# Performance work log

Hardware: AMD Instinct MI355X
Metric: run time of the kernel (lower is better)

Reference implementation:

```python
import jax, jax.numpy as jnp
import numpy as np

NEG_BIG = -9e15
ALPHA = 0.2  # LeakyReLU slope


def setup_inputs() -> dict:
    key = jax.random.key(0)
    k1, k2, k3, k4 = jax.random.split(key, 4)
    B, N, Fin, Fout = 8, 2048, 256, 64
    h = jax.random.normal(k1, (B, N, Fin), dtype=jnp.float32)
    adj = jax.random.randint(k2, (B, N, N), 0, 2, dtype=jnp.int32)
    # xavier_uniform-ish scale for W and a
    W = jax.random.normal(k3, (Fin, Fout), dtype=jnp.float32) * (1.414 * np.sqrt(2.0 / (Fin + Fout)))
    a = jax.random.normal(k4, (2 * Fout, 1), dtype=jnp.float32) * (1.414 * np.sqrt(2.0 / (2 * Fout + 1)))
    return {"h": h, "adj": adj, "W": W, "a": a}


def reference(h, adj, W, a):
    Fout = W.shape[1]
    Wh = jnp.einsum("bnf,fo->bno", h, W)  # [B,N,Fout]
    # Decompose concat-based score: a_input @ a == Wh@a1 (src) + Wh@a2 (dst)
    a1, a2 = a[:Fout, 0], a[Fout:, 0]
    e_src = Wh @ a1  # [B,N]
    e_dst = Wh @ a2  # [B,N]
    e = e_src[:, :, None] + e_dst[:, None, :]  # [B,N,N]
    e = jnp.where(e > 0, e, ALPHA * e)  # LeakyReLU
    scores = jnp.where(adj > 0, e, NEG_BIG)
    attention = jax.nn.softmax(scores, axis=-1)  # [B,N,N]
    h_prime = jnp.einsum("bnm,bmo->bno", attention, Wh)
    return jax.nn.elu(h_prime)  # concat=True
```

## Files before the change

### kernel.cpp

```cpp
#include <hip/hip_runtime.h>

#define L2E 1.44269504088896340736f

typedef float f32x4 __attribute__((ext_vector_type(4)));
typedef __bf16 bf16x8 __attribute__((ext_vector_type(8)));
typedef __bf16 bf16x4 __attribute__((ext_vector_type(4)));

__device__ inline void mfma_bf16(bf16x8 a, bf16x8 b, f32x4& c) {
    c = __builtin_amdgcn_mfma_f32_16x16x32_bf16(a, b, c, 0, 0, 0);
}


__global__ __launch_bounds__(256, 2)
void k1_wh(const float* __restrict__ h, const float* __restrict__ W,
           const float* __restrict__ a, __bf16* __restrict__ whP,
           float* __restrict__ esrc, float* __restrict__ edst) {
    const int tid  = threadIdx.x;
    const int lane = tid & 63;
    const int w    = tid >> 6;
    const int blk  = blockIdx.x;
    const int r0   = blk * 8;
    const int b    = r0 >> 11;
    const int n0   = r0 & 2047;

    __shared__ float pt_s[8][4][64];
    __shared__ float whs[64][8];

    float wreg[64];
    {
        const float* Wp = W + (size_t)(w * 64) * 64 + lane;
#pragma unroll
        for (int kk = 0; kk < 64; kk++) wreg[kk] = Wp[(size_t)kk * 64];
    }

    const float* hbase = h + (size_t)r0 * 256 + w * 64;
    for (int rr = 0; rr < 8; rr++) {
        const float4* hp = (const float4*)(hbase + rr * 256);
        float acc = 0.f;
#pragma unroll
        for (int q = 0; q < 16; q++) {
            float4 hv = hp[q];
            acc += hv.x * wreg[4 * q + 0];
            acc += hv.y * wreg[4 * q + 1];
            acc += hv.z * wreg[4 * q + 2];
            acc += hv.w * wreg[4 * q + 3];
        }
        pt_s[rr][w][lane] = acc;
    }
    __syncthreads();

    const float a1 = a[lane];
    const float a2 = a[64 + lane];
#pragma unroll
    for (int rq = 0; rq < 2; rq++) {
        const int rr = w * 2 + rq;
        float v = pt_s[rr][0][lane] + pt_s[rr][1][lane] +
                  pt_s[rr][2][lane] + pt_s[rr][3][lane];
        whs[lane][rr] = v;
        float e1 = v * a1, e2 = v * a2;
#pragma unroll
        for (int d = 1; d < 64; d <<= 1) {
            e1 += __shfl_xor(e1, d);
            e2 += __shfl_xor(e2, d);
        }
        if (lane == 0) { esrc[r0 + rr] = e1; edst[r0 + rr] = e2; }
    }
    __syncthreads();

    if (tid < 128) {
        const int o  = tid >> 1, hf = (tid & 1) * 4;
        float4 v = *(const float4*)&whs[o][hf];
        bf16x4 bv = { (__bf16)v.x, (__bf16)v.y, (__bf16)v.z, (__bf16)v.w };
        const int t   = n0 >> 6;
        const int kh  = (n0 >> 5) & 1;
        const int hi2 = (n0 >> 3) & 3;
        const int ob  = o >> 4;
        const int rr  = o & 15;
        const size_t flat =
            ((((size_t)(b * 32 + t) * 2 + kh) * 4 + ob) * 4 + hi2) * 128 +
            rr * 8 + hf;
        *(bf16x4*)(whP + flat) = bv;
    }
}

__global__ __launch_bounds__(256, 2)
void k2_attn(const int* __restrict__ adj, const __bf16* __restrict__ whP,
             const float* __restrict__ esrc, const float* __restrict__ edst,
             float* __restrict__ out) {
    const int tid  = threadIdx.x;
    const int lane = tid & 63;
    const int jg   = tid >> 6;
    const int blk  = blockIdx.x;
    const int b    = blk >> 7;
    const int i0   = (blk & 127) * 16;
    const int r    = lane & 15;
    const int hi   = lane >> 4;

    __shared__ float edst_s[2048];
    __shared__ float esrc_s[16];
    __shared__ float red_s[4];
    __shared__ unsigned msk_s[16][66];
    __shared__ float mrg_acc[3][1024];
    __shared__ float mrg_l[3][16];

#pragma unroll
    for (int rr = 0; rr < 4; rr++) {
        const int row = jg * 4 + rr;
        const int* arow = adj + (size_t)(b * 2048 + i0 + row) * 2048 + lane;
        int av[32];
#pragma unroll
        for (int k = 0; k < 32; k++) av[k] = arow[k * 64];
        unsigned myd = 0u;
#pragma unroll
        for (int k = 0; k < 32; k++) {
            unsigned long long bal = __ballot(av[k] > 0);
            if ((lane >> 1) == k)
                myd = (lane & 1) ? (unsigned)(bal >> 32) : (unsigned)bal;
        }
        msk_s[row][lane] = myd;
    }

    float mymax = -3.0e38f;
#pragma unroll
    for (int q = 0; q < 2; q++) {
        float4 v = *(const float4*)&edst[b * 2048 + q * 1024 + tid * 4];
        *(float4*)&edst_s[q * 1024 + tid * 4] = v;
        mymax = fmaxf(fmaxf(mymax, v.x), fmaxf(v.y, fmaxf(v.z, v.w)));
    }
#pragma unroll
    for (int d = 1; d < 64; d <<= 1) mymax = fmaxf(mymax, __shfl_xor(mymax, d));
    if (lane == 0) red_s[jg] = mymax;
    if (tid < 16) esrc_s[tid] = esrc[b * 2048 + i0 + tid];
    __syncthreads();

    const float maxed = fmaxf(fmaxf(red_s[0], red_s[1]), fmaxf(red_s[2], red_s[3]));
    const float es = esrc_s[r];
    float M = es + maxed;
    M = fmaxf(M, 0.2f * M);
    const float Mc = M * L2E;

    const int jbase = jg * 512;
    const __bf16* wbase = whP + (size_t)b * 131072 +
                          (size_t)(jg * 8) * 4096 + lane * 8;

    f32x4 lacc = {0.f, 0.f, 0.f, 0.f};
    f32x4 acc0 = {0.f,0.f,0.f,0.f}, acc1 = {0.f,0.f,0.f,0.f};
    f32x4 acc2 = {0.f,0.f,0.f,0.f}, acc3 = {0.f,0.f,0.f,0.f};

#define PB(E, bits, sh, base)                                                 \
    {                                                                         \
        const unsigned bb = (bits) >> (sh);                                   \
        float v;                                                              \
        v = es + E.x; v = fmaxf(v, 0.2f * v);                                 \
        p[base + 0] = (bb & 1u) ? exp2f(__builtin_fmaf(v, L2E, -Mc)) : 0.f;   \
        v = es + E.y; v = fmaxf(v, 0.2f * v);                                 \
        p[base + 1] = (bb & 2u) ? exp2f(__builtin_fmaf(v, L2E, -Mc)) : 0.f;   \
        v = es + E.z; v = fmaxf(v, 0.2f * v);                                 \
        p[base + 2] = (bb & 4u) ? exp2f(__builtin_fmaf(v, L2E, -Mc)) : 0.f;   \
        v = es + E.w; v = fmaxf(v, 0.2f * v);                                 \
        p[base + 3] = (bb & 8u) ? exp2f(__builtin_fmaf(v, L2E, -Mc)) : 0.f;   \
    }

    for (int tl = 0; tl < 8; ++tl) {
        const int jt = tl * 64;
        const uint2 m2 = *(const uint2*)&msk_s[r][jg * 16 + tl * 2];
        const unsigned blo = m2.x >> (hi * 8);
        const unsigned bhi = m2.y >> (hi * 8);
        const __bf16* wb = wbase + (size_t)tl * 4096;
        bf16x8 B00 = *(const bf16x8*)(wb);
        bf16x8 B01 = *(const bf16x8*)(wb + 512);
        bf16x8 B02 = *(const bf16x8*)(wb + 1024);
        bf16x8 B03 = *(const bf16x8*)(wb + 1536);
        bf16x8 B10 = *(const bf16x8*)(wb + 2048);
        bf16x8 B11 = *(const bf16x8*)(wb + 2560);
        bf16x8 B12 = *(const bf16x8*)(wb + 3072);
        bf16x8 B13 = *(const bf16x8*)(wb + 3584);
        float4 e0 = *(const float4*)&edst_s[jbase + jt + hi * 8];
        float4 e1 = *(const float4*)&edst_s[jbase + jt + hi * 8 + 4];
        float4 e2 = *(const float4*)&edst_s[jbase + jt + 32 + hi * 8];
        float4 e3 = *(const float4*)&edst_s[jbase + jt + 32 + hi * 8 + 4];
        float p[16];
        PB(e0, blo, 0, 0) PB(e1, blo, 4, 4) PB(e2, bhi, 0, 8) PB(e3, bhi, 4, 12)
        lacc[0] += p[0] + p[4] + p[8]  + p[12];
        lacc[1] += p[1] + p[5] + p[9]  + p[13];
        lacc[2] += p[2] + p[6] + p[10] + p[14];
        lacc[3] += p[3] + p[7] + p[11] + p[15];
        bf16x8 pa0, pa1;
#pragma unroll
        for (int e = 0; e < 8; e++) {
            pa0[e] = (__bf16)p[e];
            pa1[e] = (__bf16)p[e + 8];
        }
        mfma_bf16(pa0, B00, acc0); mfma_bf16(pa1, B10, acc0);
        mfma_bf16(pa0, B01, acc1); mfma_bf16(pa1, B11, acc1);
        mfma_bf16(pa0, B02, acc2); mfma_bf16(pa1, B12, acc2);
        mfma_bf16(pa0, B03, acc3); mfma_bf16(pa1, B13, acc3);
    }
#undef PB

    float lsum = lacc[0] + lacc[1] + lacc[2] + lacc[3];
    lsum += __shfl_xor(lsum, 16);
    lsum += __shfl_xor(lsum, 32);

    if (jg > 0) {
        float* mb = mrg_acc[jg - 1];
        *(f32x4*)&mb[lane * 4]       = acc0;
        *(f32x4*)&mb[256 + lane * 4] = acc1;
        *(f32x4*)&mb[512 + lane * 4] = acc2;
        *(f32x4*)&mb[768 + lane * 4] = acc3;
        if (lane < 16) mrg_l[jg - 1][r] = lsum;
    }
    __syncthreads();
    if (jg == 0) {
        float ltot = lsum;
#pragma unroll
        for (int wv = 0; wv < 3; wv++) {
            const float* mb = mrg_acc[wv];
            acc0 += *(const f32x4*)&mb[lane * 4];
            acc1 += *(const f32x4*)&mb[256 + lane * 4];
            acc2 += *(const f32x4*)&mb[512 + lane * 4];
            acc3 += *(const f32x4*)&mb[768 + lane * 4];
            ltot += mrg_l[wv][r];
        }
#pragma unroll
        for (int reg = 0; reg < 4; reg++) {
            const float L  = __shfl(ltot, hi * 4 + reg);
            const float iL = 1.0f / L;
            float v0 = acc0[reg] * iL;
            float v1 = acc1[reg] * iL;
            float v2 = acc2[reg] * iL;
            float v3 = acc3[reg] * iL;
            v0 = v0 > 0.f ? v0 : expm1f(v0);
            v1 = v1 > 0.f ? v1 : expm1f(v1);
            v2 = v2 > 0.f ? v2 : expm1f(v2);
            v3 = v3 > 0.f ? v3 : expm1f(v3);
            float* op = out + (size_t)(b * 2048 + i0 + hi * 4 + reg) * 64 + r;
            op[0]  = v0;
            op[16] = v1;
            op[32] = v2;
            op[48] = v3;
        }
    }
}

extern "C" void kernel_launch(void* const* d_in, const int* in_sizes, int n_in,
                              void* d_out, int out_size, void* d_ws, size_t ws_size,
                              hipStream_t stream) {
    const float* h   = (const float*)d_in[0];
    const int*   adj = (const int*)d_in[1];
    const float* W   = (const float*)d_in[2];
    const float* a   = (const float*)d_in[3];
    float* out = (float*)d_out;

    __bf16* whP  = (__bf16*)d_ws;
    float*  esrc = (float*)((char*)d_ws + (size_t)8 * 131072 * 2);
    float*  edst = esrc + 8 * 2048;

    hipLaunchKernelGGL(k1_wh, dim3(2048), dim3(256), 0, stream,
                       h, W, a, whP, esrc, edst);
    hipLaunchKernelGGL(k2_attn, dim3(1024), dim3(256), 0, stream,
                       adj, whP, esrc, edst, out);
}
```

Before: 74.60 us.

## Process 32 rows per attention block to reuse Wh fragments across two row tiles

Each attention block now handles 32 query rows instead of 16. Every loaded Wh B-fragment and edst slice feeds MFMAs for two row tiles, and the grid is halved. The cross-wave merge becomes a tree reduction through a smaller, lane-major shared buffer, and the launch bound asks for 3 blocks per CU. The aim is to halve redundant Wh/L2 traffic per output row, but it raises register pressure and leaves only 512 blocks, which may underfill the GPU.

```diff
diff --git a/kernel.cpp b/kernel.cpp
--- a/kernel.cpp
+++ b/kernel.cpp
@@ -83,7 +83,7 @@
     }
 }
 
-__global__ __launch_bounds__(256, 2)
+__global__ __launch_bounds__(256, 3)
 void k2_attn(const int* __restrict__ adj, const __bf16* __restrict__ whP,
              const float* __restrict__ esrc, const float* __restrict__ edst,
              float* __restrict__ out) {
@@ -91,21 +91,21 @@
     const int lane = tid & 63;
     const int jg   = tid >> 6;
     const int blk  = blockIdx.x;
-    const int b    = blk >> 7;
-    const int i0   = (blk & 127) * 16;
+    const int b    = blk & 7;
+    const int i0   = (blk >> 3) * 32;
     const int r    = lane & 15;
     const int hi   = lane >> 4;
 
     __shared__ float edst_s[2048];
-    __shared__ float esrc_s[16];
+    __shared__ float esrc_s[32];
     __shared__ float red_s[4];
-    __shared__ unsigned msk_s[16][66];
-    __shared__ float mrg_acc[3][1024];
-    __shared__ float mrg_l[3][16];
-
-#pragma unroll
-    for (int rr = 0; rr < 4; rr++) {
-        const int row = jg * 4 + rr;
+    __shared__ unsigned msk_s[32][66];
+    __shared__ float mrg_s[2][8][4][64];
+    __shared__ float mrgl_s[2][2][16];
+
+#pragma unroll
+    for (int rr = 0; rr < 8; rr++) {
+        const int row = jg * 8 + rr;
         const int* arow = adj + (size_t)(b * 2048 + i0 + row) * 2048 + lane;
         int av[32];
 #pragma unroll
@@ -130,42 +130,47 @@
 #pragma unroll
     for (int d = 1; d < 64; d <<= 1) mymax = fmaxf(mymax, __shfl_xor(mymax, d));
     if (lane == 0) red_s[jg] = mymax;
-    if (tid < 16) esrc_s[tid] = esrc[b * 2048 + i0 + tid];
+    if (tid < 32) esrc_s[tid] = esrc[b * 2048 + i0 + tid];
     __syncthreads();
 
     const float maxed = fmaxf(fmaxf(red_s[0], red_s[1]), fmaxf(red_s[2], red_s[3]));
-    const float es = esrc_s[r];
-    float M = es + maxed;
-    M = fmaxf(M, 0.2f * M);
-    const float Mc = M * L2E;
+    const float es0 = esrc_s[r];
+    const float es1 = esrc_s[16 + r];
+    float M0 = es0 + maxed; M0 = fmaxf(M0, 0.2f * M0);
+    float M1 = es1 + maxed; M1 = fmaxf(M1, 0.2f * M1);
+    const float Mc0 = M0 * L2E;
+    const float Mc1 = M1 * L2E;
 
     const int jbase = jg * 512;
     const __bf16* wbase = whP + (size_t)b * 131072 +
                           (size_t)(jg * 8) * 4096 + lane * 8;
 
-    f32x4 lacc = {0.f, 0.f, 0.f, 0.f};
-    f32x4 acc0 = {0.f,0.f,0.f,0.f}, acc1 = {0.f,0.f,0.f,0.f};
-    f32x4 acc2 = {0.f,0.f,0.f,0.f}, acc3 = {0.f,0.f,0.f,0.f};
-
-#define PB(E, bits, sh, base)                                                 \
+    f32x4 laccA = {0,0,0,0}, laccB = {0,0,0,0};
+    f32x4 accA0={0,0,0,0}, accA1={0,0,0,0}, accA2={0,0,0,0}, accA3={0,0,0,0};
+    f32x4 accB0={0,0,0,0}, accB1={0,0,0,0}, accB2={0,0,0,0}, accB3={0,0,0,0};
+
+#define PB(ES, MC, E, bits, sh, base)                                         \
     {                                                                         \
         const unsigned bb = (bits) >> (sh);                                   \
         float v;                                                              \
-        v = es + E.x; v = fmaxf(v, 0.2f * v);                                 \
-        p[base + 0] = (bb & 1u) ? exp2f(__builtin_fmaf(v, L2E, -Mc)) : 0.f;   \
-        v = es + E.y; v = fmaxf(v, 0.2f * v);                                 \
-        p[base + 1] = (bb & 2u) ? exp2f(__builtin_fmaf(v, L2E, -Mc)) : 0.f;   \
-        v = es + E.z; v = fmaxf(v, 0.2f * v);                                 \
-        p[base + 2] = (bb & 4u) ? exp2f(__builtin_fmaf(v, L2E, -Mc)) : 0.f;   \
-        v = es + E.w; v = fmaxf(v, 0.2f * v);                                 \
-        p[base + 3] = (bb & 8u) ? exp2f(__builtin_fmaf(v, L2E, -Mc)) : 0.f;   \
+        v = (ES) + E.x; v = fmaxf(v, 0.2f * v);                               \
+        p[base + 0] = (bb & 1u) ? exp2f(__builtin_fmaf(v, L2E, -(MC))) : 0.f; \
+        v = (ES) + E.y; v = fmaxf(v, 0.2f * v);                               \
+        p[base + 1] = (bb & 2u) ? exp2f(__builtin_fmaf(v, L2E, -(MC))) : 0.f; \
+        v = (ES) + E.z; v = fmaxf(v, 0.2f * v);                               \
+        p[base + 2] = (bb & 4u) ? exp2f(__builtin_fmaf(v, L2E, -(MC))) : 0.f; \
+        v = (ES) + E.w; v = fmaxf(v, 0.2f * v);                               \
+        p[base + 3] = (bb & 8u) ? exp2f(__builtin_fmaf(v, L2E, -(MC))) : 0.f; \
     }
 
     for (int tl = 0; tl < 8; ++tl) {
         const int jt = tl * 64;
-        const uint2 m2 = *(const uint2*)&msk_s[r][jg * 16 + tl * 2];
-        const unsigned blo = m2.x >> (hi * 8);
-        const unsigned bhi = m2.y >> (hi * 8);
+        const uint2 mA = *(const uint2*)&msk_s[r][jg * 16 + tl * 2];
+        const uint2 mB = *(const uint2*)&msk_s[16 + r][jg * 16 + tl * 2];
+        const unsigned aLo = mA.x >> (hi * 8);
+        const unsigned aHi = mA.y >> (hi * 8);
+        const unsigned bLo = mB.x >> (hi * 8);
+        const unsigned bHi = mB.y >> (hi * 8);
         const __bf16* wb = wbase + (size_t)tl * 4096;
         bf16x8 B00 = *(const bf16x8*)(wb);
         bf16x8 B01 = *(const bf16x8*)(wb + 512);
@@ -180,67 +185,109 @@
         float4 e2 = *(const float4*)&edst_s[jbase + jt + 32 + hi * 8];
         float4 e3 = *(const float4*)&edst_s[jbase + jt + 32 + hi * 8 + 4];
         float p[16];
-        PB(e0, blo, 0, 0) PB(e1, blo, 4, 4) PB(e2, bhi, 0, 8) PB(e3, bhi, 4, 12)
-        lacc[0] += p[0] + p[4] + p[8]  + p[12];
-        lacc[1] += p[1] + p[5] + p[9]  + p[13];
-        lacc[2] += p[2] + p[6] + p[10] + p[14];
-        lacc[3] += p[3] + p[7] + p[11] + p[15];
-        bf16x8 pa0, pa1;
+        PB(es0, Mc0, e0, aLo, 0, 0)  PB(es0, Mc0, e1, aLo, 4, 4)
+        PB(es0, Mc0, e2, aHi, 0, 8)  PB(es0, Mc0, e3, aHi, 4, 12)
+        laccA[0] += p[0] + p[4] + p[8]  + p[12];
+        laccA[1] += p[1] + p[5] + p[9]  + p[13];
+        laccA[2] += p[2] + p[6] + p[10] + p[14];
+        laccA[3] += p[3] + p[7] + p[11] + p[15];
+        bf16x8 paA0, paA1;
 #pragma unroll
         for (int e = 0; e < 8; e++) {
-            pa0[e] = (__bf16)p[e];
-            pa1[e] = (__bf16)p[e + 8];
-        }
-        mfma_bf16(pa0, B00, acc0); mfma_bf16(pa1, B10, acc0);
-        mfma_bf16(pa0, B01, acc1); mfma_bf16(pa1, B11, acc1);
-        mfma_bf16(pa0, B02, acc2); mfma_bf16(pa1, B12, acc2);
-        mfma_bf16(pa0, B03, acc3); mfma_bf16(pa1, B13, acc3);
+            paA0[e] = (__bf16)p[e];
+            paA1[e] = (__bf16)p[e + 8];
+        }
+        PB(es1, Mc1, e0, bLo, 0, 0)  PB(es1, Mc1, e1, bLo, 4, 4)
+        PB(es1, Mc1, e2, bHi, 0, 8)  PB(es1, Mc1, e3, bHi, 4, 12)
+        laccB[0] += p[0] + p[4] + p[8]  + p[12];
+        laccB[1] += p[1] + p[5] + p[9]  + p[13];
+        laccB[2] += p[2] + p[6] + p[10] + p[14];
+        laccB[3] += p[3] + p[7] + p[11] + p[15];
+        bf16x8 paB0, paB1;
+#pragma unroll
+        for (int e = 0; e < 8; e++) {
+            paB0[e] = (__bf16)p[e];
+            paB1[e] = (__bf16)p[e + 8];
+        }
+        mfma_bf16(paA0, B00, accA0); mfma_bf16(paA1, B10, accA0);
+        mfma_bf16(paA0, B01, accA1); mfma_bf16(paA1, B11, accA1);
+        mfma_bf16(paA0, B02, accA2); mfma_bf16(paA1, B12, accA2);
+        mfma_bf16(paA0, B03, accA3); mfma_bf16(paA1, B13, accA3);
+        mfma_bf16(paB0, B00, accB0); mfma_bf16(paB1, B10, accB0);
+        mfma_bf16(paB0, B01, accB1); mfma_bf16(paB1, B11, accB1);
+        mfma_bf16(paB0, B02, accB2); mfma_bf16(paB1, B12, accB2);
+        mfma_bf16(paB0, B03, accB3); mfma_bf16(paB1, B13, accB3);
     }
 #undef PB
 
-    float lsum = lacc[0] + lacc[1] + lacc[2] + lacc[3];
-    lsum += __shfl_xor(lsum, 16);
-    lsum += __shfl_xor(lsum, 32);
-
-    if (jg > 0) {
-        float* mb = mrg_acc[jg - 1];
-        *(f32x4*)&mb[lane * 4]       = acc0;
-        *(f32x4*)&mb[256 + lane * 4] = acc1;
-        *(f32x4*)&mb[512 + lane * 4] = acc2;
-        *(f32x4*)&mb[768 + lane * 4] = acc3;
-        if (lane < 16) mrg_l[jg - 1][r] = lsum;
-    }
+    float lsA = laccA[0] + laccA[1] + laccA[2] + laccA[3];
+    lsA += __shfl_xor(lsA, 16); lsA += __shfl_xor(lsA, 32);
+    float lsB = laccB[0] + laccB[1] + laccB[2] + laccB[3];
+    lsB += __shfl_xor(lsB, 16); lsB += __shfl_xor(lsB, 32);
+
+#define ST_ACC(Rg)                                                            \
+    {                                                                         \
+        _Pragma("unroll")                                                     \
+        for (int reg = 0; reg < 4; reg++) {                                   \
+            mrg_s[Rg][0][reg][lane] = accA0[reg];                             \
+            mrg_s[Rg][1][reg][lane] = accA1[reg];                             \
+            mrg_s[Rg][2][reg][lane] = accA2[reg];                             \
+            mrg_s[Rg][3][reg][lane] = accA3[reg];                             \
+            mrg_s[Rg][4][reg][lane] = accB0[reg];                             \
+            mrg_s[Rg][5][reg][lane] = accB1[reg];                             \
+            mrg_s[Rg][6][reg][lane] = accB2[reg];                             \
+            mrg_s[Rg][7][reg][lane] = accB3[reg];                             \
+        }                                                                     \
+        if (lane < 16) { mrgl_s[Rg][0][r] = lsA; mrgl_s[Rg][1][r] = lsB; }    \
+    }
+
+#define ADD_ACC(Rg)                                                           \
+    {                                                                         \
+        _Pragma("unroll")                                                     \
+        for (int reg = 0; reg < 4; reg++) {                                   \
+            accA0[reg] += mrg_s[Rg][0][reg][lane];                            \
+            accA1[reg] += mrg_s[Rg][1][reg][lane];                            \
+            accA2[reg] += mrg_s[Rg][2][reg][lane];                            \
+            accA3[reg] += mrg_s[Rg][3][reg][lane];                            \
+            accB0[reg] += mrg_s[Rg][4][reg][lane];                            \
+            accB1[reg] += mrg_s[Rg][5][reg][lane];                            \
+            accB2[reg] += mrg_s[Rg][6][reg][lane];                            \
+            accB3[reg] += mrg_s[Rg][7][reg][lane];                            \
+        }                                                                     \
+        lsA += mrgl_s[Rg][0][r]; lsB += mrgl_s[Rg][1][r];                     \
+    }
+
+    if (jg == 1) ST_ACC(0)
+    if (jg == 3) ST_ACC(1)
+    __syncthreads();
+    if (jg == 0) ADD_ACC(0)
+    if (jg == 2) ADD_ACC(1)
+    __syncthreads();
+    if (jg == 2) ST_ACC(0)
     __syncthreads();
     if (jg == 0) {
-        float ltot = lsum;
-#pragma unroll
-        for (int wv = 0; wv < 3; wv++) {
-            const float* mb = mrg_acc[wv];
-            acc0 += *(const f32x4*)&mb[lane * 4];
-            acc1 += *(const f32x4*)&mb[256 + lane * 4];
-            acc2 += *(const f32x4*)&mb[512 + lane * 4];
-            acc3 += *(const f32x4*)&mb[768 + lane * 4];
-            ltot += mrg_l[wv][r];
-        }
+        ADD_ACC(0)
 #pragma unroll
         for (int reg = 0; reg < 4; reg++) {
-            const float L  = __shfl(ltot, hi * 4 + reg);
-            const float iL = 1.0f / L;
-            float v0 = acc0[reg] * iL;
-            float v1 = acc1[reg] * iL;
-            float v2 = acc2[reg] * iL;
-            float v3 = acc3[reg] * iL;
-            v0 = v0 > 0.f ? v0 : expm1f(v0);
-            v1 = v1 > 0.f ? v1 : expm1f(v1);
-            v2 = v2 > 0.f ? v2 : expm1f(v2);
-            v3 = v3 > 0.f ? v3 : expm1f(v3);
-            float* op = out + (size_t)(b * 2048 + i0 + hi * 4 + reg) * 64 + r;
-            op[0]  = v0;
-            op[16] = v1;
-            op[32] = v2;
-            op[48] = v3;
-        }
-    }
+            const float LA  = __shfl(lsA, hi * 4 + reg);
+            const float LB  = __shfl(lsB, hi * 4 + reg);
+            const float iLA = 1.0f / LA;
+            const float iLB = 1.0f / LB;
+            float* opA = out + (size_t)(b * 2048 + i0 + hi * 4 + reg) * 64 + r;
+            float* opB = opA + 16 * 64;
+            float v;
+            v = accA0[reg] * iLA; v = v > 0.f ? v : expm1f(v); opA[0]  = v;
+            v = accA1[reg] * iLA; v = v > 0.f ? v : expm1f(v); opA[16] = v;
+            v = accA2[reg] * iLA; v = v > 0.f ? v : expm1f(v); opA[32] = v;
+            v = accA3[reg] * iLA; v = v > 0.f ? v : expm1f(v); opA[48] = v;
+            v = accB0[reg] * iLB; v = v > 0.f ? v : expm1f(v); opB[0]  = v;
+            v = accB1[reg] * iLB; v = v > 0.f ? v : expm1f(v); opB[16] = v;
+            v = accB2[reg] * iLB; v = v > 0.f ? v : expm1f(v); opB[32] = v;
+            v = accB3[reg] * iLB; v = v > 0.f ? v : expm1f(v); opB[48] = v;
+        }
+    }
+#undef ST_ACC
+#undef ADD_ACC
 }
 
 extern "C" void kernel_launch(void* const* d_in, const int* in_sizes, int n_in,
@@ -258,6 +305,6 @@
 
     hipLaunchKernelGGL(k1_wh, dim3(2048), dim3(256), 0, stream,
                        h, W, a, whP, esrc, edst);
-    hipLaunchKernelGGL(k2_attn, dim3(1024), dim3(256), 0, stream,
+    hipLaunchKernelGGL(k2_attn, dim3(512), dim3(256), 0, stream,
                        adj, whP, esrc, edst, out);
 }
```

Measured after the change: 80.25 us. 1.08x slower.
